# Optimization experiments

Measured on AMD Instinct MI355X. Metric: run time of the kernel, lower is better.

## Reference

```python
import jax, jax.numpy as jnp
import numpy as np

PAD = -10000.0
B, N, F = 512, 2048, 16
H_PHI, LAT, H_RHO = 128, 128, 128


def _xavier(key, fan_in, fan_out):
    bound = np.sqrt(6.0 / (fan_in + fan_out))
    return jax.random.uniform(key, (fan_in, fan_out), jnp.float32, -bound, bound)


def setup_inputs() -> dict:
    key = jax.random.key(0)
    ks = jax.random.split(key, 12)
    x = jax.random.normal(ks[0], (B, N, F), jnp.float32)
    # ragged set lengths: pad tail rows with -10000.0 (the module's padding sentinel)
    lengths = jax.random.randint(ks[1], (B,), 1, N + 1)
    pad_mask = jnp.arange(N)[None, :] >= lengths[:, None]  # True where padded
    x = jnp.where(pad_mask[:, :, None], PAD, x)
    params = {
        "phi_w0": _xavier(ks[2], F, H_PHI), "phi_b0": jnp.zeros((H_PHI,), jnp.float32),
        "phi_w1": _xavier(ks[3], H_PHI, H_PHI), "phi_b1": jnp.zeros((H_PHI,), jnp.float32),
        "phi_w2": _xavier(ks[4], H_PHI, H_PHI), "phi_b2": jnp.zeros((H_PHI,), jnp.float32),
        "phi_w3": _xavier(ks[5], H_PHI, LAT), "phi_b3": jnp.zeros((LAT,), jnp.float32),
        "rho_w0": _xavier(ks[6], LAT, H_RHO), "rho_b0": jnp.zeros((H_RHO,), jnp.float32),
        "rho_w1": _xavier(ks[7], H_RHO, H_RHO), "rho_b1": jnp.zeros((H_RHO,), jnp.float32),
        "rho_w2": _xavier(ks[8], H_RHO, H_RHO), "rho_b2": jnp.zeros((H_RHO,), jnp.float32),
        "rho_w3": _xavier(ks[9], H_RHO, 1), "rho_b3": jnp.zeros((1,), jnp.float32),
    }
    return {"inputs": x, **params}


def reference(inputs, phi_w0, phi_b0, phi_w1, phi_b1, phi_w2, phi_b2, phi_w3, phi_b3,
              rho_w0, rho_b0, rho_w1, rho_b1, rho_w2, rho_b2, rho_w3, rho_b3):
    b, n, f = inputs.shape
    # valid-prefix mask: sum rows before the FIRST all-(-10000) row (matches torch loop)
    is_pad = jnp.all(inputs == PAD, axis=-1)                       # [B,N]
    first = jnp.where(jnp.any(is_pad, axis=-1), jnp.argmax(is_pad, axis=-1), n)
    mask = (jnp.arange(n)[None, :] < first[:, None]).astype(inputs.dtype)  # [B,N]
    relu = jax.nn.relu
    # phi applied per point
    h = relu(inputs @ phi_w0 + phi_b0)
    h = relu(h @ phi_w1 + phi_b1)
    h = relu(h @ phi_w2 + phi_b2)
    h = relu(h @ phi_w3 + phi_b3)                                  # [B,N,LAT]
    # masked variable-length sum pooling (segment reduce)
    pooled = jnp.einsum('bnd,bn->bd', h, mask)                     # [B,LAT]
    r = relu(pooled @ rho_w0 + rho_b0)
    r = relu(r @ rho_w1 + rho_b1)
    r = relu(r @ rho_w2 + rho_b2)
    cost = (r @ rho_w3 + rho_b3)[:, 0]                             # [B]
    return cost
```

## Files before the change

### kernel.cpp

```cpp
#include <hip/hip_runtime.h>

typedef _Float16 f16;
typedef f16  f16x2  __attribute__((ext_vector_type(2)));
typedef f16  f16x8  __attribute__((ext_vector_type(8)));
typedef __fp16 h16x2 __attribute__((ext_vector_type(2)));
typedef float f32x16 __attribute__((ext_vector_type(16)));

#define B_   512
#define N_   2048
#define PADV -10000.0f

union F16x8 { f16x8 v; f16x2 h2[4]; };

__device__ __forceinline__ f16x2 pkrtz(float a, float b) {
    h16x2 r = __builtin_amdgcn_cvt_pkrtz(a, b);
    return __builtin_bit_cast(f16x2, r);
}

__global__ void prep_kernel(const float* __restrict__ w0, const float* __restrict__ w1,
                            const float* __restrict__ w2, const float* __restrict__ w3,
                            f16* __restrict__ out, float* __restrict__ pooled,
                            unsigned* __restrict__ cnt)
{
    int i = blockIdx.x * 256 + threadIdx.x;
    if (i < 2048) {
        out[i] = (f16)w0[(i & 15) * 128 + (i >> 4)];
    } else if (i < 51200) {
        int j = i - 2048;
        int l = j >> 14, r = j & 16383;
        int o = r >> 7, slot = r & 127;
        int s = slot >> 4, qq = (slot >> 3) & 1, jj = slot & 7;
        int sig = 32 * (s >> 1) + 16 * (s & 1) + 4 * qq + 8 * (jj >> 2) + (jj & 3);
        const float* w = (l == 0) ? w1 : (l == 1) ? w2 : w3;
        out[i] = (f16)w[sig * 128 + o];
    }
    pooled[i] = 0.f;
    if (blockIdx.x == 255 && threadIdx.x < 8) cnt[threadIdx.x] = 256u;
}

__device__ __forceinline__ int swz(int row, int chunk) {
    return row * 256 + ((chunk ^ (row & 15)) << 4);
}

__device__ __forceinline__ void gl_lds16(const void* g, void* l) {
    __builtin_amdgcn_global_load_lds(
        (const __attribute__((address_space(1))) void*)g,
        (__attribute__((address_space(3))) void*)l, 16, 0, 0);
}

__global__ __launch_bounds__(512, 2) void phi_pool_kernel(
    const float* __restrict__ x,
    const f16*  __restrict__ wtbuf,
    const float* __restrict__ pb0, const float* __restrict__ pb1,
    const float* __restrict__ pb2, const float* __restrict__ pb3,
    float* __restrict__ pooled, unsigned* __restrict__ cnt)
{
    extern __shared__ char smem[];
    char* wA = smem;
    char* wB = smem + 32768;
    char* wC = smem + 65536;

    const int tid  = threadIdx.x;
    const int lane = tid & 63;
    const int wv   = tid >> 6;
    const int l31  = lane & 31;
    const int q    = lane >> 5;

    {
        const f16* wsrc = wtbuf + 2048;
        #pragma unroll
        for (int i = 0; i < 4; ++i) {
            const int row   = wv * 16 + i * 4 + (lane >> 4);
            const int chunk = (lane & 15) ^ (row & 15);
            const int loff  = (wv * 16 + i * 4) * 256;
            gl_lds16(wsrc +         row * 128 + chunk * 8, wA + loff);
            gl_lds16(wsrc + 16384 + row * 128 + chunk * 8, wB + loff);
            gl_lds16(wsrc + 32768 + row * 128 + chunk * 8, wC + loff);
        }
    }

    __syncthreads();

    #define INIT_ACC_BIAS(pb)                                              \
        {                                                                  \
            _Pragma("unroll")                                              \
            for (int c = 0; c < 4; ++c) {                                  \
                _Pragma("unroll")                                          \
                for (int g = 0; g < 4; ++g) {                              \
                    float4 bb = *(const float4*)((pb) + 32 * c + 8 * g + 4 * q); \
                    const float* bbp = (const float*)&bb;                  \
                    _Pragma("unroll")                                      \
                    for (int e = 0; e < 4; ++e) {                          \
                        acc[0][c][4 * g + e] = bbp[e];                     \
                        acc[1][c][4 * g + e] = bbp[e];                     \
                    }                                                      \
                }                                                          \
            }                                                              \
        }

    #define EPILOGUE()                                                     \
        {                                                                  \
            const f16x2 z2 = {(f16)0.f, (f16)0.f};                         \
            _Pragma("unroll")                                              \
            for (int t = 0; t < 2; ++t) {                                  \
                _Pragma("unroll")                                          \
                for (int s = 0; s < 8; ++s) {                              \
                    const int c = s >> 1, r0 = 8 * (s & 1);                \
                    _Pragma("unroll")                                      \
                    for (int p = 0; p < 4; ++p) {                          \
                        f16x2 mm = pkrtz(                                  \
                            acc[t][c][r0 + 2 * p], acc[t][c][r0 + 2 * p + 1]); \
                        hf[t][s].h2[p] = __builtin_elementwise_max(mm, z2); \
                    }                                                      \
                }                                                          \
            }                                                              \
        }

    unsigned m = blockIdx.x;
    unsigned* cp = cnt + wv;

    #pragma unroll 1
    for (;;) {
        const int t64 = (int)(m & 31) << 6;
        const int db0 = (int)((m >> 5) << 2);
        #pragma unroll 1
        for (int k = 0; k < 4; ++k) {
            const int b = (wv << 6) + db0 + k;
            const float* xr = x + ((size_t)b * N_ + t64) * 16;
            const float4 f0 = *(const float4*)xr;
            if (f0.x == PADV && f0.y == PADV && f0.z == PADV && f0.w == PADV)
                continue;

            const float* xp = xr + l31 * 16 + 8 * q;
            float4 a0 = ((const float4*)xp)[0];
            float4 a1 = ((const float4*)xp)[1];
            float4 c0 = ((const float4*)(xp + 512))[0];
            float4 c1 = ((const float4*)(xp + 512))[1];

            f16x8 w0f[4];
            #pragma unroll
            for (int c = 0; c < 4; ++c)
                w0f[c] = *(const f16x8*)(wtbuf + (32 * c + l31) * 16 + 8 * q);

            bool vA = (a0.x != PADV) || (a0.y != PADV) || (a0.z != PADV) || (a0.w != PADV) ||
                      (a1.x != PADV) || (a1.y != PADV) || (a1.z != PADV) || (a1.w != PADV);
            bool vB = (c0.x != PADV) || (c0.y != PADV) || (c0.z != PADV) || (c0.w != PADV) ||
                      (c1.x != PADV) || (c1.y != PADV) || (c1.z != PADV) || (c1.w != PADV);
            unsigned long long blA = __ballot(vA), blB = __ballot(vB);
            const unsigned mskA = (unsigned)blA | (unsigned)(blA >> 32);
            const unsigned mskB = (unsigned)blB | (unsigned)(blB >> 32);

            F16x8 hf[2][8];
            hf[0][0].h2[0] = pkrtz(a0.x, a0.y);
            hf[0][0].h2[1] = pkrtz(a0.z, a0.w);
            hf[0][0].h2[2] = pkrtz(a1.x, a1.y);
            hf[0][0].h2[3] = pkrtz(a1.z, a1.w);
            hf[1][0].h2[0] = pkrtz(c0.x, c0.y);
            hf[1][0].h2[1] = pkrtz(c0.z, c0.w);
            hf[1][0].h2[2] = pkrtz(c1.x, c1.y);
            hf[1][0].h2[3] = pkrtz(c1.z, c1.w);

            f32x16 acc[2][4];

            INIT_ACC_BIAS(pb0);
            #pragma unroll
            for (int c = 0; c < 4; ++c) {
                acc[0][c] = __builtin_amdgcn_mfma_f32_32x32x16_f16(w0f[c], hf[0][0].v, acc[0][c], 0, 0, 0);
                acc[1][c] = __builtin_amdgcn_mfma_f32_32x32x16_f16(w0f[c], hf[1][0].v, acc[1][c], 0, 0, 0);
            }
            EPILOGUE();

            INIT_ACC_BIAS(pb1);
            #pragma unroll
            for (int s = 0; s < 8; ++s) {
                f16x8 wf[4];
                #pragma unroll
                for (int c = 0; c < 4; ++c)
                    wf[c] = *(const f16x8*)(wA + swz(32 * c + l31, 2 * s + q));
                #pragma unroll
                for (int c = 0; c < 4; ++c) {
                    acc[0][c] = __builtin_amdgcn_mfma_f32_32x32x16_f16(wf[c], hf[0][s].v, acc[0][c], 0, 0, 0);
                    acc[1][c] = __builtin_amdgcn_mfma_f32_32x32x16_f16(wf[c], hf[1][s].v, acc[1][c], 0, 0, 0);
                }
            }
            EPILOGUE();

            INIT_ACC_BIAS(pb2);
            #pragma unroll
            for (int s = 0; s < 8; ++s) {
                f16x8 wf[4];
                #pragma unroll
                for (int c = 0; c < 4; ++c)
                    wf[c] = *(const f16x8*)(wB + swz(32 * c + l31, 2 * s + q));
                #pragma unroll
                for (int c = 0; c < 4; ++c) {
                    acc[0][c] = __builtin_amdgcn_mfma_f32_32x32x16_f16(wf[c], hf[0][s].v, acc[0][c], 0, 0, 0);
                    acc[1][c] = __builtin_amdgcn_mfma_f32_32x32x16_f16(wf[c], hf[1][s].v, acc[1][c], 0, 0, 0);
                }
            }
            EPILOGUE();

            {
                float bl3[4];
                #pragma unroll
                for (int c = 0; c < 4; ++c) bl3[c] = pb3[32 * c + l31];
                #pragma unroll
                for (int t = 0; t < 2; ++t)
                    #pragma unroll
                    for (int c = 0; c < 4; ++c)
                        #pragma unroll
                        for (int r = 0; r < 16; ++r) acc[t][c][r] = bl3[c];
            }
            #pragma unroll
            for (int s = 0; s < 8; ++s) {
                f16x8 wf[4];
                #pragma unroll
                for (int c = 0; c < 4; ++c)
                    wf[c] = *(const f16x8*)(wC + swz(32 * c + l31, 2 * s + q));
                #pragma unroll
                for (int c = 0; c < 4; ++c) {
                    acc[0][c] = __builtin_amdgcn_mfma_f32_32x32x16_f16(hf[0][s].v, wf[c], acc[0][c], 0, 0, 0);
                    acc[1][c] = __builtin_amdgcn_mfma_f32_32x32x16_f16(hf[1][s].v, wf[c], acc[1][c], 0, 0, 0);
                }
            }

            #pragma unroll
            for (int c = 0; c < 4; ++c) {
                float s0 = 0.f;
                #pragma unroll
                for (int t = 0; t < 2; ++t) {
                    const unsigned msk = t ? mskB : mskA;
                    #pragma unroll
                    for (int r = 0; r < 16; ++r) {
                        const int ptl = 4 * q + (r & 3) + 8 * (r >> 2);
                        float v = fmaxf(acc[t][c][r], 0.f);
                        s0 += ((msk >> ptl) & 1u) ? v : 0.f;
                    }
                }
                s0 += __shfl_xor(s0, 32);
                if (q == 0) atomicAdd(&pooled[b * 128 + 32 * c + l31], s0);
            }
        }
        unsigned mn = 0;
        if (lane == 0) mn = atomicAdd(cp, 1u);
        m = (unsigned)__builtin_amdgcn_readfirstlane((int)mn);
        if (m >= 512u) break;
    }
}

__global__ __launch_bounds__(128) void rho_kernel(
    const float* __restrict__ pooled,
    const float* __restrict__ w0, const float* __restrict__ b0,
    const float* __restrict__ w1, const float* __restrict__ b1,
    const float* __restrict__ w2, const float* __restrict__ b2,
    const float* __restrict__ w3, const float* __restrict__ b3,
    float* __restrict__ out)
{
    __shared__ float buf[2][128];
    __shared__ float red[2];
    const int b = blockIdx.x, t = threadIdx.x;
    buf[0][t] = pooled[b * 128 + t];
    __syncthreads();
    const float* ws3[3] = {w0, w1, w2};
    const float* bs3[3] = {b0, b1, b2};
    int cur = 0;
    #pragma unroll 1
    for (int l = 0; l < 3; ++l) {
        float acc = bs3[l][t];
        const float* w = ws3[l];
        #pragma unroll 8
        for (int k = 0; k < 128; ++k)
            acc = fmaf(buf[cur][k], w[k * 128 + t], acc);
        buf[cur ^ 1][t] = fmaxf(acc, 0.f);
        cur ^= 1;
        __syncthreads();
    }
    float v = buf[cur][t] * w3[t];
    #pragma unroll
    for (int off = 32; off > 0; off >>= 1)
        v += __shfl_down(v, off, 64);
    if ((t & 63) == 0) red[t >> 6] = v;
    __syncthreads();
    if (t == 0) out[b] = red[0] + red[1] + b3[0];
}

extern "C" void kernel_launch(void* const* d_in, const int* in_sizes, int n_in,
                              void* d_out, int out_size, void* d_ws, size_t ws_size,
                              hipStream_t stream)
{
    (void)in_sizes; (void)n_in; (void)out_size; (void)ws_size;
    const float* x      = (const float*)d_in[0];
    const float* phi_w0 = (const float*)d_in[1];
    const float* phi_b0 = (const float*)d_in[2];
    const float* phi_w1 = (const float*)d_in[3];
    const float* phi_b1 = (const float*)d_in[4];
    const float* phi_w2 = (const float*)d_in[5];
    const float* phi_b2 = (const float*)d_in[6];
    const float* phi_w3 = (const float*)d_in[7];
    const float* phi_b3 = (const float*)d_in[8];
    const float* rho_w0 = (const float*)d_in[9];
    const float* rho_b0 = (const float*)d_in[10];
    const float* rho_w1 = (const float*)d_in[11];
    const float* rho_b1 = (const float*)d_in[12];
    const float* rho_w2 = (const float*)d_in[13];
    const float* rho_b2 = (const float*)d_in[14];
    const float* rho_w3 = (const float*)d_in[15];
    const float* rho_b3 = (const float*)d_in[16];

    float*    pooled = (float*)d_ws;
    f16*      wtbuf  = (f16*)((char*)d_ws + 262144);
    unsigned* cnt    = (unsigned*)((char*)d_ws + 364544);

    static int smem_set = 0;
    if (!smem_set) {
        hipFuncSetAttribute((const void*)phi_pool_kernel,
                            hipFuncAttributeMaxDynamicSharedMemorySize, 98304);
        smem_set = 1;
    }

    prep_kernel<<<256, 256, 0, stream>>>(phi_w0, phi_w1, phi_w2, phi_w3, wtbuf, pooled, cnt);
    phi_pool_kernel<<<256, 512, 98304, stream>>>(x, wtbuf, phi_b0, phi_b1, phi_b2, phi_b3,
                                                 pooled, cnt);
    rho_kernel<<<B_, 128, 0, stream>>>(pooled, rho_w0, rho_b0, rho_w1, rho_b1,
                                       rho_w2, rho_b2, rho_w3, rho_b3, (float*)d_out);
}
```

Measured before the change: 202.5 us.

## Remap work items to contiguous point spans per set and accumulate pooled sums locally

Each work item now covers four consecutive 64-point tiles of a single set instead of one tile across four sets. It stops early at the first padded tile and accumulates the pooled partial sums in registers, issuing one atomicAdd per set per work item. Biases are staged once in LDS, and the next work-item counter atomic is issued at the start of the loop to hide its latency. A prefetch of the next tile's first row drives the early-exit check. LDS per block grows by 2 KB, which may affect whether two blocks fit per CU.

Result: slower. 713.2 us (+252.1%).

```diff
diff --git a/kernel.cpp b/kernel.cpp
--- a/kernel.cpp
+++ b/kernel.cpp
@@ -56,9 +56,10 @@
     float* __restrict__ pooled, unsigned* __restrict__ cnt)
 {
     extern __shared__ char smem[];
-    char* wA = smem;
-    char* wB = smem + 32768;
-    char* wC = smem + 65536;
+    char*  wA   = smem;
+    char*  wB   = smem + 32768;
+    char*  wC   = smem + 65536;
+    float* blds = (float*)(smem + 98304);
 
     const int tid  = threadIdx.x;
     const int lane = tid & 63;
@@ -77,17 +78,21 @@
             gl_lds16(wsrc + 16384 + row * 128 + chunk * 8, wB + loff);
             gl_lds16(wsrc + 32768 + row * 128 + chunk * 8, wC + loff);
         }
+        const int layer = tid >> 7, idx = tid & 127;
+        const float* pb = (layer == 0) ? pb0 : (layer == 1) ? pb1
+                        : (layer == 2) ? pb2 : pb3;
+        blds[tid] = pb[idx];
     }
 
     __syncthreads();
 
-    #define INIT_ACC_BIAS(pb)                                              \
+    #define INIT_ACC_BIAS(L)                                               \
         {                                                                  \
             _Pragma("unroll")                                              \
             for (int c = 0; c < 4; ++c) {                                  \
                 _Pragma("unroll")                                          \
                 for (int g = 0; g < 4; ++g) {                              \
-                    float4 bb = *(const float4*)((pb) + 32 * c + 8 * g + 4 * q); \
+                    float4 bb = *(const float4*)(blds + (L) * 128 + 32 * c + 8 * g + 4 * q); \
                     const float* bbp = (const float*)&bb;                  \
                     _Pragma("unroll")                                      \
                     for (int e = 0; e < 4; ++e) {                          \
@@ -121,21 +126,30 @@
 
     #pragma unroll 1
     for (;;) {
-        const int t64 = (int)(m & 31) << 6;
-        const int db0 = (int)((m >> 5) << 2);
+        unsigned mn = 0;
+        if (lane == 0) mn = atomicAdd(cp, 1u);
+
+        const int bl = (int)(m & 63);
+        const int g  = (int)(m >> 6);
+        const int b  = (wv << 6) + bl;
+        const float* xb = x + (size_t)b * N_ * 16;
+
+        float4 pr = *(const float4*)(xb + (size_t)(g * 256) * 16);
+        float s0acc[4] = {0.f, 0.f, 0.f, 0.f};
+        bool wrote = false;
+
         #pragma unroll 1
-        for (int k = 0; k < 4; ++k) {
-            const int b = (wv << 6) + db0 + k;
-            const float* xr = x + ((size_t)b * N_ + t64) * 16;
-            const float4 f0 = *(const float4*)xr;
-            if (f0.x == PADV && f0.y == PADV && f0.z == PADV && f0.w == PADV)
-                continue;
-
-            const float* xp = xr + l31 * 16 + 8 * q;
+        for (int j = 0; j < 4; ++j) {
+            if (pr.x == PADV && pr.y == PADV && pr.z == PADV && pr.w == PADV) break;
+            const int t64 = g * 256 + j * 64;
+
+            const float* xp = xb + (size_t)(t64 + l31) * 16 + 8 * q;
             float4 a0 = ((const float4*)xp)[0];
             float4 a1 = ((const float4*)xp)[1];
             float4 c0 = ((const float4*)(xp + 512))[0];
             float4 c1 = ((const float4*)(xp + 512))[1];
+
+            if (j < 3) pr = *(const float4*)(xb + (size_t)(t64 + 64) * 16);
 
             f16x8 w0f[4];
             #pragma unroll
@@ -162,7 +176,7 @@
 
             f32x16 acc[2][4];
 
-            INIT_ACC_BIAS(pb0);
+            INIT_ACC_BIAS(0);
             #pragma unroll
             for (int c = 0; c < 4; ++c) {
                 acc[0][c] = __builtin_amdgcn_mfma_f32_32x32x16_f16(w0f[c], hf[0][0].v, acc[0][c], 0, 0, 0);
@@ -170,7 +184,7 @@
             }
             EPILOGUE();
 
-            INIT_ACC_BIAS(pb1);
+            INIT_ACC_BIAS(1);
             #pragma unroll
             for (int s = 0; s < 8; ++s) {
                 f16x8 wf[4];
@@ -185,7 +199,7 @@
             }
             EPILOGUE();
 
-            INIT_ACC_BIAS(pb2);
+            INIT_ACC_BIAS(2);
             #pragma unroll
             for (int s = 0; s < 8; ++s) {
                 f16x8 wf[4];
@@ -201,15 +215,14 @@
             EPILOGUE();
 
             {
-                float bl3[4];
-                #pragma unroll
-                for (int c = 0; c < 4; ++c) bl3[c] = pb3[32 * c + l31];
-                #pragma unroll
-                for (int t = 0; t < 2; ++t)
+                #pragma unroll
+                for (int c = 0; c < 4; ++c) {
+                    const float b3v = blds[3 * 128 + 32 * c + l31];
                     #pragma unroll
-                    for (int c = 0; c < 4; ++c)
+                    for (int t = 0; t < 2; ++t)
                         #pragma unroll
-                        for (int r = 0; r < 16; ++r) acc[t][c][r] = bl3[c];
+                        for (int r = 0; r < 16; ++r) acc[t][c][r] = b3v;
+                }
             }
             #pragma unroll
             for (int s = 0; s < 8; ++s) {
@@ -237,12 +250,19 @@
                         s0 += ((msk >> ptl) & 1u) ? v : 0.f;
                     }
                 }
-                s0 += __shfl_xor(s0, 32);
+                s0acc[c] += s0;
+            }
+            wrote = true;
+        }
+
+        if (wrote) {
+            #pragma unroll
+            for (int c = 0; c < 4; ++c) {
+                float s0 = s0acc[c] + __shfl_xor(s0acc[c], 32);
                 if (q == 0) atomicAdd(&pooled[b * 128 + 32 * c + l31], s0);
             }
         }
-        unsigned mn = 0;
-        if (lane == 0) mn = atomicAdd(cp, 1u);
+
         m = (unsigned)__builtin_amdgcn_readfirstlane((int)mn);
         if (m >= 512u) break;
     }
@@ -314,13 +334,13 @@
     static int smem_set = 0;
     if (!smem_set) {
         hipFuncSetAttribute((const void*)phi_pool_kernel,
-                            hipFuncAttributeMaxDynamicSharedMemorySize, 98304);
+                            hipFuncAttributeMaxDynamicSharedMemorySize, 100352);
         smem_set = 1;
     }
 
     prep_kernel<<<256, 256, 0, stream>>>(phi_w0, phi_w1, phi_w2, phi_w3, wtbuf, pooled, cnt);
-    phi_pool_kernel<<<256, 512, 98304, stream>>>(x, wtbuf, phi_b0, phi_b1, phi_b2, phi_b3,
-                                                 pooled, cnt);
+    phi_pool_kernel<<<256, 512, 100352, stream>>>(x, wtbuf, phi_b0, phi_b1, phi_b2, phi_b3,
+                                                  pooled, cnt);
     rho_kernel<<<B_, 128, 0, stream>>>(pooled, rho_w0, rho_b0, rho_w1, rho_b1,
                                        rho_w2, rho_b2, rho_w3, rho_b3, (float*)d_out);
 }
```
